# Performance work log

Hardware: AMD Instinct MI355X
Metric: run time of the kernel (lower is better)

## Reference

```python
import jax, jax.numpy as jnp
import numpy as np
from jax import lax

B, H, G, T = 16384, 128, 5, 12

def setup_inputs() -> dict:
    key = jax.random.key(0)
    ks = jax.random.split(key, 12)
    s = 0.05  # weight scale for numerical sanity
    return {
        "encoder_hidden": jax.random.normal(ks[0], (B, H), jnp.float32),
        "encoder_cell": jax.random.normal(ks[1], (B, H), jnp.float32),
        "last_position": jax.random.normal(ks[2], (B, 2), jnp.float32),
        "gp_w1": jax.random.normal(ks[3], (H, H), jnp.float32) * s,
        "gp_b1": jnp.zeros((H,), jnp.float32),
        "gp_w2": jax.random.normal(ks[4], (H, G * 2), jnp.float32) * s,
        "gp_b2": jnp.zeros((G * 2,), jnp.float32),
        "pr_w1": jax.random.normal(ks[5], (H, H // 2), jnp.float32) * s,
        "pr_b1": jnp.zeros((H // 2,), jnp.float32),
        "pr_w2": jax.random.normal(ks[6], (H // 2, G), jnp.float32) * s,
        "pr_b2": jnp.zeros((G,), jnp.float32),
        "w_ih": jax.random.normal(ks[7], (4, 4 * H), jnp.float32) * s,   # LSTM input weights [in=4, 4H] (i,f,g,o)
        "w_hh": jax.random.normal(ks[8], (H, 4 * H), jnp.float32) * s,   # LSTM recurrent weights [H, 4H]
        "b_ih": jnp.zeros((4 * H,), jnp.float32),
        "b_hh": jnp.zeros((4 * H,), jnp.float32),
        "ph_w": jax.random.normal(ks[9], (H, 2), jnp.float32) * s,
        "ph_b": jnp.zeros((2,), jnp.float32),
    }

def reference(encoder_hidden, encoder_cell, last_position,
              gp_w1, gp_b1, gp_w2, gp_b2,
              pr_w1, pr_b1, pr_w2, pr_b2,
              w_ih, w_hh, b_ih, b_hh, ph_w, ph_b):
    b = encoder_hidden.shape[0]
    # goal prediction: residual on last_position
    g_hid = jax.nn.relu(encoder_hidden @ gp_w1 + gp_b1)
    goals = (g_hid @ gp_w2 + gp_b2).reshape(b, G, 2) + last_position[:, None, :]  # [B,G,2]
    # goal probabilities
    p_hid = jax.nn.relu(encoder_hidden @ pr_w1 + pr_b1)
    goal_probs = jax.nn.softmax(p_hid @ pr_w2 + pr_b2, axis=-1)  # [B,G]
    # batch all goals together: leading goal dim [G,B,...]
    goals_gb = jnp.swapaxes(goals, 0, 1)                      # [G,B,2]
    h0 = jnp.broadcast_to(encoder_hidden, (G, b, H))
    c0 = jnp.broadcast_to(encoder_cell, (G, b, H))
    pos0 = jnp.broadcast_to(last_position, (G, b, 2))
    bias = b_ih + b_hh

    def step(carry, _):
        pos, h, c = carry
        x = jnp.concatenate([pos, goals_gb], axis=-1)          # [G,B,4]
        gates = x @ w_ih + h @ w_hh + bias                      # [G,B,4H]
        i, f, g, o = jnp.split(gates, 4, axis=-1)
        c_new = jax.nn.sigmoid(f) * c + jax.nn.sigmoid(i) * jnp.tanh(g)
        h_new = jax.nn.sigmoid(o) * jnp.tanh(c_new)
        pos_new = pos + (h_new @ ph_w + ph_b)                   # residual position update
        return (pos_new, h_new, c_new), pos_new

    _, path = lax.scan(step, (pos0, h0, c0), None, length=T)   # [T,G,B,2]
    predictions = jnp.transpose(path, (2, 1, 0, 3))            # [B,G,T,2]
    return predictions, goals, goal_probs
```

## Files before the change

### kernel.cpp

```cpp
#include <hip/hip_runtime.h>

#define Bn 16384
#define Hn 128
#define Gn 5
#define Tn 12

typedef __attribute__((ext_vector_type(8))) __bf16 bf16x8;
typedef __attribute__((ext_vector_type(4))) float f32x4;
typedef __attribute__((ext_vector_type(4))) unsigned int u32x4;
typedef __attribute__((ext_vector_type(2))) unsigned int u32x2;
typedef unsigned int u32;
typedef unsigned short u16;

#define MFMA(a, b, c) __builtin_amdgcn_mfma_f32_16x16x32_bf16((a), (b), (c), 0, 0, 0)

__device__ __forceinline__ u16 f2bf(float f) { return __builtin_bit_cast(u16, (__bf16)f); }
__device__ __forceinline__ float bf2f(u16 h) { u32 u = ((u32)h) << 16; return __builtin_bit_cast(float, u); }
__device__ __forceinline__ u32 pk2(float a, float b) { return (u32)f2bf(a) | ((u32)f2bf(b) << 16); }
__device__ __forceinline__ float sigf(float x) {
    return __builtin_amdgcn_rcpf(1.0f + __builtin_amdgcn_exp2f(-1.44269504f * x));
}
__device__ __forceinline__ float tanhf_(float x) {
    return 1.0f - 2.0f * __builtin_amdgcn_rcpf(1.0f + __builtin_amdgcn_exp2f(2.88539008f * x));
}

__device__ __forceinline__ int hbsw(int row, int bytein) {
    return row * 256 + ((((bytein >> 4) ^ row) & 15) << 4) + (bytein & 15);
}
__device__ __forceinline__ int pbsw(int row, int bytein) {
    return row * 128 + ((((bytein >> 4) ^ row) & 7) << 4) + (bytein & 15);
}

__global__ __launch_bounds__(256) void k_phaseA(
    const float* __restrict__ eh, const float* __restrict__ lastpos,
    const float* __restrict__ gp_w1, const float* __restrict__ gp_b1,
    const float* __restrict__ gp_w2, const float* __restrict__ gp_b2,
    const float* __restrict__ pr_w1, const float* __restrict__ pr_b1,
    const float* __restrict__ pr_w2, const float* __restrict__ pr_b2,
    float* __restrict__ goals_o, float* __restrict__ probs_o)
{
    __shared__ __align__(16) char eT[64 * 256];
    __shared__ __align__(16) char gT[64 * 256];
    __shared__ __align__(16) char pT[64 * 128];
    __shared__ float lgT[64 * 8];

    const int tid = threadIdx.x;
    const int lane = tid & 63;
    const int wv = tid >> 6;
    const int lg = lane >> 4, li = lane & 15;
    const int r0 = blockIdx.x * 64;
    const int rowbase = wv * 16;

    {
        int row = tid >> 2, seg = tid & 3;
        const float* src = eh + (size_t)(r0 + row) * Hn + seg * 32;
#pragma unroll
        for (int cc = 0; cc < 4; ++cc) {
            u32 p0 = pk2(src[cc * 8 + 0], src[cc * 8 + 1]);
            u32 p1 = pk2(src[cc * 8 + 2], src[cc * 8 + 3]);
            u32 p2 = pk2(src[cc * 8 + 4], src[cc * 8 + 5]);
            u32 p3 = pk2(src[cc * 8 + 6], src[cc * 8 + 7]);
            *(u32x4*)(eT + hbsw(row, seg * 64 + cc * 16)) = (u32x4){p0, p1, p2, p3};
        }
    }
    __syncthreads();

    bf16x8 Ae[4];
#pragma unroll
    for (int kc = 0; kc < 4; ++kc)
        Ae[kc] = *(const bf16x8*)(eT + hbsw(rowbase + li, kc * 64 + lg * 16));

#pragma unroll 1
    for (int nt = 0; nt < 8; ++nt) {
        int c1 = nt * 16 + li;
        f32x4 acc = {0.f, 0.f, 0.f, 0.f};
#pragma unroll
        for (int kc = 0; kc < 4; ++kc) {
            bf16x8 bfr;
#pragma unroll
            for (int j = 0; j < 8; ++j)
                bfr[j] = (__bf16)gp_w1[(size_t)(kc * 32 + lg * 8 + j) * Hn + c1];
            acc = MFMA(Ae[kc], bfr, acc);
        }
        float bias = gp_b1[c1];
#pragma unroll
        for (int r = 0; r < 4; ++r) {
            int row = rowbase + lg * 4 + r;
            float v = fmaxf(acc[r] + bias, 0.f);
            *(u16*)(gT + hbsw(row, c1 * 2)) = f2bf(v);
        }
    }
    __syncthreads();

    {
        bf16x8 Ag[4];
#pragma unroll
        for (int kc = 0; kc < 4; ++kc)
            Ag[kc] = *(const bf16x8*)(gT + hbsw(rowbase + li, kc * 64 + lg * 16));
        f32x4 acc = {0.f, 0.f, 0.f, 0.f};
#pragma unroll
        for (int kc = 0; kc < 4; ++kc) {
            bf16x8 bfr;
#pragma unroll
            for (int j = 0; j < 8; ++j) {
                int k = kc * 32 + lg * 8 + j;
                bfr[j] = (li < 10) ? (__bf16)gp_w2[k * 10 + li] : (__bf16)0.f;
            }
            acc = MFMA(Ag[kc], bfr, acc);
        }
        if (li < 10) {
            float b2 = gp_b2[li];
#pragma unroll
            for (int r = 0; r < 4; ++r) {
                int b = r0 + rowbase + lg * 4 + r;
                float v = acc[r] + b2 + lastpos[(size_t)b * 2 + (li & 1)];
                goals_o[(size_t)b * 10 + li] = v;
            }
        }
    }

#pragma unroll 1
    for (int nt = 0; nt < 4; ++nt) {
        int c1 = nt * 16 + li;
        f32x4 acc = {0.f, 0.f, 0.f, 0.f};
#pragma unroll
        for (int kc = 0; kc < 4; ++kc) {
            bf16x8 bfr;
#pragma unroll
            for (int j = 0; j < 8; ++j)
                bfr[j] = (__bf16)pr_w1[(size_t)(kc * 32 + lg * 8 + j) * 64 + c1];
            acc = MFMA(Ae[kc], bfr, acc);
        }
        float bias = pr_b1[c1];
#pragma unroll
        for (int r = 0; r < 4; ++r) {
            int row = rowbase + lg * 4 + r;
            float v = fmaxf(acc[r] + bias, 0.f);
            *(u16*)(pT + pbsw(row, c1 * 2)) = f2bf(v);
        }
    }
    __syncthreads();

    {
        bf16x8 Ap[2];
#pragma unroll
        for (int kc = 0; kc < 2; ++kc)
            Ap[kc] = *(const bf16x8*)(pT + pbsw(rowbase + li, kc * 64 + lg * 16));
        f32x4 acc = {0.f, 0.f, 0.f, 0.f};
#pragma unroll
        for (int kc = 0; kc < 2; ++kc) {
            bf16x8 bfr;
#pragma unroll
            for (int j = 0; j < 8; ++j) {
                int k = kc * 32 + lg * 8 + j;
                bfr[j] = (li < 5) ? (__bf16)pr_w2[k * 5 + li] : (__bf16)0.f;
            }
            acc = MFMA(Ap[kc], bfr, acc);
        }
        if (li < 5) {
            float b2 = pr_b2[li];
#pragma unroll
            for (int r = 0; r < 4; ++r) {
                int row = rowbase + lg * 4 + r;
                lgT[row * 8 + li] = acc[r] + b2;
            }
        }
    }
    __syncthreads();

    if (tid < 64) {
        int row = tid;
        float v0 = lgT[row * 8 + 0], v1 = lgT[row * 8 + 1], v2 = lgT[row * 8 + 2];
        float v3 = lgT[row * 8 + 3], v4 = lgT[row * 8 + 4];
        float mx = fmaxf(fmaxf(fmaxf(v0, v1), fmaxf(v2, v3)), v4);
        float e0 = __builtin_amdgcn_exp2f((v0 - mx) * 1.44269504f);
        float e1 = __builtin_amdgcn_exp2f((v1 - mx) * 1.44269504f);
        float e2 = __builtin_amdgcn_exp2f((v2 - mx) * 1.44269504f);
        float e3 = __builtin_amdgcn_exp2f((v3 - mx) * 1.44269504f);
        float e4 = __builtin_amdgcn_exp2f((v4 - mx) * 1.44269504f);
        float rs = __builtin_amdgcn_rcpf(e0 + e1 + e2 + e3 + e4);
        size_t ob = (size_t)(r0 + row) * 5;
        probs_o[ob + 0] = e0 * rs;
        probs_o[ob + 1] = e1 * rs;
        probs_o[ob + 2] = e2 * rs;
        probs_o[ob + 3] = e3 * rs;
        probs_o[ob + 4] = e4 * rs;
    }
}

__global__ __launch_bounds__(512) void k_lstm(
    const float* __restrict__ eh, const float* __restrict__ ec,
    const float* __restrict__ lastpos,
    const float* __restrict__ w_ih, const float* __restrict__ w_hh,
    const float* __restrict__ b_ih, const float* __restrict__ b_hh,
    const float* __restrict__ ph_w, const float* __restrict__ ph_b,
    const float* __restrict__ goals_o, float* __restrict__ preds)
{
    __shared__ __align__(16) char hT[2][64 * 256];

    const int tid = threadIdx.x;
    const int lane = tid & 63;
    const int wv = tid >> 6;
    const int lg = lane >> 4, li = lane & 15;
    const int r0 = blockIdx.x * 64;

    bf16x8 Wh[4][4];
    bf16x8 Wx[4];
#pragma unroll
    for (int gt = 0; gt < 4; ++gt) {
        const int cg = gt * 128 + wv * 16 + li;
#pragma unroll
        for (int kc = 0; kc < 4; ++kc) {
            bf16x8 f;
#pragma unroll
            for (int j = 0; j < 8; ++j)
                f[j] = (__bf16)w_hh[(size_t)(kc * 32 + lg * 8 + j) * 512 + cg];
            Wh[gt][kc] = f;
        }
        bf16x8 fx;
#pragma unroll
        for (int j = 0; j < 8; ++j) {
            int k = lg * 8 + j;
            float v = 0.f;
            if (k < 4) v = w_ih[k * 512 + cg];
            else if (k == 4) v = b_ih[cg] + b_hh[cg];
            fx[j] = (__bf16)v;
        }
        Wx[gt] = fx;
    }

    bf16x8 php[4];
#pragma unroll
    for (int kc = 0; kc < 4; ++kc) {
        u32 w[4];
#pragma unroll
        for (int jp = 0; jp < 4; ++jp) {
            int k = kc * 32 + lg * 8 + jp * 2;
            u32 xw = pk2(ph_w[k * 2 + 0], ph_w[k * 2 + 2]);
            u32 yw = pk2(ph_w[k * 2 + 1], ph_w[k * 2 + 3]);
            w[jp] = (li == 0) ? xw : yw;
        }
        php[kc] = __builtin_bit_cast(bf16x8, (u32x4){w[0], w[1], w[2], w[3]});
    }
    const float phb0 = ph_b[0], phb1 = ph_b[1];

    u32 gpk[4];
    float px[4], py[4];
#pragma unroll
    for (int m = 0; m < 4; ++m) {
        int gr = r0 + m * 16 + li;
        float2 g2 = *(const float2*)(goals_o + (size_t)gr * 2);
        gpk[m] = pk2(g2.x, g2.y);
        float2 p = *(const float2*)(lastpos + (size_t)(gr / 5) * 2);
        px[m] = p.x; py[m] = p.y;
    }

    const int ro0 = hbsw(li, 0 + lg * 16);
    const int ro1 = hbsw(li, 64 + lg * 16);
    const int ro2 = hbsw(li, 128 + lg * 16);
    const int ro3 = hbsw(li, 192 + lg * 16);
    const int wo  = hbsw(li, wv * 32 + lg * 8);

    {
        int row = tid >> 3, seg = tid & 7;
        int b = (r0 + row) / 5;
        const float* src = eh + (size_t)b * Hn + seg * 16;
#pragma unroll
        for (int cp = 0; cp < 2; ++cp) {
            u32 p0 = pk2(src[cp * 8 + 0], src[cp * 8 + 1]);
            u32 p1 = pk2(src[cp * 8 + 2], src[cp * 8 + 3]);
            u32 p2 = pk2(src[cp * 8 + 4], src[cp * 8 + 5]);
            u32 p3 = pk2(src[cp * 8 + 6], src[cp * 8 + 7]);
            *(u32x4*)(hT[0] + hbsw(row, seg * 32 + cp * 16)) = (u32x4){p0, p1, p2, p3};
        }
    }

    float c[4][4];
#pragma unroll
    for (int m = 0; m < 4; ++m) {
        int b = (r0 + m * 16 + li) / 5;
        float4 cv = *(const float4*)(ec + (size_t)b * Hn + wv * 16 + lg * 4);
        c[m][0] = cv.x; c[m][1] = cv.y; c[m][2] = cv.z; c[m][3] = cv.w;
    }

    __syncthreads();

#pragma unroll 1
    for (int t = 0; t < Tn; ++t) {
        const char* rbp = hT[0] + (t & 1) * 16384;
        char* wbp = hT[0] + ((t & 1) ^ 1) * 16384;
#pragma unroll
        for (int m = 0; m < 4; ++m) {
            const int mo = m * 4096;
            bf16x8 H0 = *(const bf16x8*)(rbp + ro0 + mo);
            bf16x8 H1 = *(const bf16x8*)(rbp + ro1 + mo);
            bf16x8 H2 = *(const bf16x8*)(rbp + ro2 + mo);
            bf16x8 H3 = *(const bf16x8*)(rbp + ro3 + mo);

            f32x4 a0 = {0.f, 0.f, 0.f, 0.f}, a1 = {0.f, 0.f, 0.f, 0.f};
            f32x4 a2 = {0.f, 0.f, 0.f, 0.f}, a3 = {0.f, 0.f, 0.f, 0.f};
            a0 = MFMA(Wh[0][0], H0, a0); a1 = MFMA(Wh[1][0], H0, a1);
            a2 = MFMA(Wh[2][0], H0, a2); a3 = MFMA(Wh[3][0], H0, a3);
            a0 = MFMA(Wh[0][1], H1, a0); a1 = MFMA(Wh[1][1], H1, a1);
            a2 = MFMA(Wh[2][1], H1, a2); a3 = MFMA(Wh[3][1], H1, a3);
            a0 = MFMA(Wh[0][2], H2, a0); a1 = MFMA(Wh[1][2], H2, a1);
            a2 = MFMA(Wh[2][2], H2, a2); a3 = MFMA(Wh[3][2], H2, a3);
            a0 = MFMA(Wh[0][3], H3, a0); a1 = MFMA(Wh[1][3], H3, a1);
            a2 = MFMA(Wh[2][3], H3, a2); a3 = MFMA(Wh[3][3], H3, a3);

            if (t > 0) {
                f32x4 pacc = {0.f, 0.f, 0.f, 0.f};
                pacc = MFMA(php[0], H0, pacc);
                pacc = MFMA(php[1], H1, pacc);
                pacc = MFMA(php[2], H2, pacc);
                pacc = MFMA(php[3], H3, pacc);
                px[m] += pacc[0] + phb0;
                py[m] += pacc[1] + phb1;
                if (wv == m && lg == 0) {
                    size_t o = ((size_t)(r0 + m * 16 + li) * Tn + (t - 1)) * 2;
                    *(float2*)(preds + o) = make_float2(px[m], py[m]);
                }
            }

            bf16x8 xf = __builtin_bit_cast(bf16x8,
                (u32x4){pk2(px[m], py[m]), gpk[m], 0x00003F80u, 0u});
            a0 = MFMA(Wx[0], xf, a0);
            a1 = MFMA(Wx[1], xf, a1);
            a2 = MFMA(Wx[2], xf, a2);
            a3 = MFMA(Wx[3], xf, a3);

            u32 w0, w1;
            {
                float cn0 = sigf(a1[0]) * c[m][0] + sigf(a0[0]) * tanhf_(a2[0]);
                float cn1 = sigf(a1[1]) * c[m][1] + sigf(a0[1]) * tanhf_(a2[1]);
                float cn2 = sigf(a1[2]) * c[m][2] + sigf(a0[2]) * tanhf_(a2[2]);
                float cn3 = sigf(a1[3]) * c[m][3] + sigf(a0[3]) * tanhf_(a2[3]);
                c[m][0] = cn0; c[m][1] = cn1; c[m][2] = cn2; c[m][3] = cn3;
                float h0 = sigf(a3[0]) * tanhf_(cn0);
                float h1 = sigf(a3[1]) * tanhf_(cn1);
                float h2 = sigf(a3[2]) * tanhf_(cn2);
                float h3 = sigf(a3[3]) * tanhf_(cn3);
                w0 = pk2(h0, h1);
                w1 = pk2(h2, h3);
            }
            *(u32x2*)(wbp + wo + mo) = (u32x2){w0, w1};
        }
        __syncthreads();
    }

    if (wv < 4) {
        const int m = wv;
        const char* rbp = hT[0];
        const int mo = m * 4096;
        bf16x8 H0 = *(const bf16x8*)(rbp + ro0 + mo);
        bf16x8 H1 = *(const bf16x8*)(rbp + ro1 + mo);
        bf16x8 H2 = *(const bf16x8*)(rbp + ro2 + mo);
        bf16x8 H3 = *(const bf16x8*)(rbp + ro3 + mo);
        f32x4 pacc = {0.f, 0.f, 0.f, 0.f};
        pacc = MFMA(php[0], H0, pacc);
        pacc = MFMA(php[1], H1, pacc);
        pacc = MFMA(php[2], H2, pacc);
        pacc = MFMA(php[3], H3, pacc);
        if (lg == 0) {
            float fx = px[m] + pacc[0] + phb0;
            float fy = py[m] + pacc[1] + phb1;
            size_t o = ((size_t)(r0 + m * 16 + li) * Tn + (Tn - 1)) * 2;
            *(float2*)(preds + o) = make_float2(fx, fy);
        }
    }
}

extern "C" void kernel_launch(void* const* d_in, const int* in_sizes, int n_in,
                              void* d_out, int out_size, void* d_ws, size_t ws_size,
                              hipStream_t stream)
{
    (void)in_sizes; (void)n_in; (void)out_size; (void)d_ws; (void)ws_size;
    const float* eh   = (const float*)d_in[0];
    const float* ec   = (const float*)d_in[1];
    const float* lp   = (const float*)d_in[2];
    const float* gpw1 = (const float*)d_in[3];
    const float* gpb1 = (const float*)d_in[4];
    const float* gpw2 = (const float*)d_in[5];
    const float* gpb2 = (const float*)d_in[6];
    const float* prw1 = (const float*)d_in[7];
    const float* prb1 = (const float*)d_in[8];
    const float* prw2 = (const float*)d_in[9];
    const float* prb2 = (const float*)d_in[10];
    const float* wih  = (const float*)d_in[11];
    const float* whh  = (const float*)d_in[12];
    const float* bih  = (const float*)d_in[13];
    const float* bhh  = (const float*)d_in[14];
    const float* phw  = (const float*)d_in[15];
    const float* phb  = (const float*)d_in[16];

    float* out = (float*)d_out;
    float* preds = out;
    float* goals = out + (size_t)Bn * Gn * Tn * 2;
    float* probs = out + (size_t)Bn * Gn * Tn * 2 + (size_t)Bn * Gn * 2;

    k_phaseA<<<Bn / 64, 256, 0, stream>>>(eh, lp, gpw1, gpb1, gpw2, gpb2,
                                          prw1, prb1, prw2, prb2, goals, probs);
    k_lstm<<<(Bn * Gn) / 64, 512, 0, stream>>>(eh, ec, lp, wih, whh, bih, bhh,
                                               phw, phb, goals, preds);
}
```

Before: 265.2 us.

## Enlarge LSTM block to 160 rows and fold activation scales into weights

Each LSTM block now processes 10 row tiles (160 rows) instead of 4. This amortizes the per-block register loading of W_hh/W_ih and cuts the block count from 1280 to 512. The log2e-based exponent scaling for the sigmoid and tanh gates is pre-multiplied into the bf16 weights and bias, removing a multiply per activation. The tradeoffs are more shared memory (80KB), which lowers occupancy, more registers for the c state, fewer blocks per CU, and a small bf16 rounding change from the scaled weights.

```diff
diff --git a/kernel.cpp b/kernel.cpp
--- a/kernel.cpp
+++ b/kernel.cpp
@@ -15,14 +15,7 @@
 #define MFMA(a, b, c) __builtin_amdgcn_mfma_f32_16x16x32_bf16((a), (b), (c), 0, 0, 0)
 
 __device__ __forceinline__ u16 f2bf(float f) { return __builtin_bit_cast(u16, (__bf16)f); }
-__device__ __forceinline__ float bf2f(u16 h) { u32 u = ((u32)h) << 16; return __builtin_bit_cast(float, u); }
 __device__ __forceinline__ u32 pk2(float a, float b) { return (u32)f2bf(a) | ((u32)f2bf(b) << 16); }
-__device__ __forceinline__ float sigf(float x) {
-    return __builtin_amdgcn_rcpf(1.0f + __builtin_amdgcn_exp2f(-1.44269504f * x));
-}
-__device__ __forceinline__ float tanhf_(float x) {
-    return 1.0f - 2.0f * __builtin_amdgcn_rcpf(1.0f + __builtin_amdgcn_exp2f(2.88539008f * x));
-}
 
 __device__ __forceinline__ int hbsw(int row, int bytein) {
     return row * 256 + ((((bytein >> 4) ^ row) & 15) << 4) + (bytein & 15);
@@ -196,25 +189,32 @@
     const float* __restrict__ ph_w, const float* __restrict__ ph_b,
     const float* __restrict__ goals_o, float* __restrict__ preds)
 {
-    __shared__ __align__(16) char hT[2][64 * 256];
+#define MT 10
+#define ROWS (MT * 16)
+#define BUFB (ROWS * 256)
+    __shared__ __align__(16) char hT[2][BUFB];
 
     const int tid = threadIdx.x;
     const int lane = tid & 63;
     const int wv = tid >> 6;
     const int lg = lane >> 4, li = lane & 15;
-    const int r0 = blockIdx.x * 64;
+    const int r0 = blockIdx.x * ROWS;
+
+    const float NL = -1.44269504f;
+    const float PG = 2.88539008f;
 
     bf16x8 Wh[4][4];
     bf16x8 Wx[4];
 #pragma unroll
     for (int gt = 0; gt < 4; ++gt) {
+        const float s = (gt == 2) ? PG : NL;
         const int cg = gt * 128 + wv * 16 + li;
 #pragma unroll
         for (int kc = 0; kc < 4; ++kc) {
             bf16x8 f;
 #pragma unroll
             for (int j = 0; j < 8; ++j)
-                f[j] = (__bf16)w_hh[(size_t)(kc * 32 + lg * 8 + j) * 512 + cg];
+                f[j] = (__bf16)(w_hh[(size_t)(kc * 32 + lg * 8 + j) * 512 + cg] * s);
             Wh[gt][kc] = f;
         }
         bf16x8 fx;
@@ -222,8 +222,8 @@
         for (int j = 0; j < 8; ++j) {
             int k = lg * 8 + j;
             float v = 0.f;
-            if (k < 4) v = w_ih[k * 512 + cg];
-            else if (k == 4) v = b_ih[cg] + b_hh[cg];
+            if (k < 4) v = w_ih[k * 512 + cg] * s;
+            else if (k == 4) v = (b_ih[cg] + b_hh[cg]) * s;
             fx[j] = (__bf16)v;
         }
         Wx[gt] = fx;
@@ -244,10 +244,10 @@
     }
     const float phb0 = ph_b[0], phb1 = ph_b[1];
 
-    u32 gpk[4];
-    float px[4], py[4];
-#pragma unroll
-    for (int m = 0; m < 4; ++m) {
+    u32 gpk[MT];
+    float px[MT], py[MT];
+#pragma unroll
+    for (int m = 0; m < MT; ++m) {
         int gr = r0 + m * 16 + li;
         float2 g2 = *(const float2*)(goals_o + (size_t)gr * 2);
         gpk[m] = pk2(g2.x, g2.y);
@@ -261,36 +261,34 @@
     const int ro3 = hbsw(li, 192 + lg * 16);
     const int wo  = hbsw(li, wv * 32 + lg * 8);
 
-    {
-        int row = tid >> 3, seg = tid & 7;
-        int b = (r0 + row) / 5;
-        const float* src = eh + (size_t)b * Hn + seg * 16;
-#pragma unroll
-        for (int cp = 0; cp < 2; ++cp) {
-            u32 p0 = pk2(src[cp * 8 + 0], src[cp * 8 + 1]);
-            u32 p1 = pk2(src[cp * 8 + 2], src[cp * 8 + 3]);
-            u32 p2 = pk2(src[cp * 8 + 4], src[cp * 8 + 5]);
-            u32 p3 = pk2(src[cp * 8 + 6], src[cp * 8 + 7]);
-            *(u32x4*)(hT[0] + hbsw(row, seg * 32 + cp * 16)) = (u32x4){p0, p1, p2, p3};
-        }
-    }
-
-    float c[4][4];
-#pragma unroll
-    for (int m = 0; m < 4; ++m) {
+#pragma unroll
+    for (int it = 0; it < 5; ++it) {
+        int chunk = tid + it * 512;
+        int row = chunk >> 4, seg = chunk & 15;
+        const float* src = eh + (size_t)((r0 + row) / 5) * Hn + seg * 8;
+        u32 p0 = pk2(src[0], src[1]);
+        u32 p1 = pk2(src[2], src[3]);
+        u32 p2 = pk2(src[4], src[5]);
+        u32 p3 = pk2(src[6], src[7]);
+        *(u32x4*)(hT[0] + hbsw(row, seg * 16)) = (u32x4){p0, p1, p2, p3};
+    }
+
+    f32x4 c[MT];
+#pragma unroll
+    for (int m = 0; m < MT; ++m) {
         int b = (r0 + m * 16 + li) / 5;
         float4 cv = *(const float4*)(ec + (size_t)b * Hn + wv * 16 + lg * 4);
-        c[m][0] = cv.x; c[m][1] = cv.y; c[m][2] = cv.z; c[m][3] = cv.w;
+        c[m] = (f32x4){cv.x, cv.y, cv.z, cv.w};
     }
 
     __syncthreads();
 
 #pragma unroll 1
     for (int t = 0; t < Tn; ++t) {
-        const char* rbp = hT[0] + (t & 1) * 16384;
-        char* wbp = hT[0] + ((t & 1) ^ 1) * 16384;
-#pragma unroll
-        for (int m = 0; m < 4; ++m) {
+        const char* rbp = hT[0] + (t & 1) * BUFB;
+        char* wbp = hT[0] + ((t & 1) ^ 1) * BUFB;
+#pragma unroll
+        for (int m = 0; m < MT; ++m) {
             const int mo = m * 4096;
             bf16x8 H0 = *(const bf16x8*)(rbp + ro0 + mo);
             bf16x8 H1 = *(const bf16x8*)(rbp + ro1 + mo);
@@ -316,7 +314,7 @@
                 pacc = MFMA(php[3], H3, pacc);
                 px[m] += pacc[0] + phb0;
                 py[m] += pacc[1] + phb1;
-                if (wv == m && lg == 0) {
+                if (((m & 7) == wv) && lg == 0) {
                     size_t o = ((size_t)(r0 + m * 16 + li) * Tn + (t - 1)) * 2;
                     *(float2*)(preds + o) = make_float2(px[m], py[m]);
                 }
@@ -331,25 +329,29 @@
 
             u32 w0, w1;
             {
-                float cn0 = sigf(a1[0]) * c[m][0] + sigf(a0[0]) * tanhf_(a2[0]);
-                float cn1 = sigf(a1[1]) * c[m][1] + sigf(a0[1]) * tanhf_(a2[1]);
-                float cn2 = sigf(a1[2]) * c[m][2] + sigf(a0[2]) * tanhf_(a2[2]);
-                float cn3 = sigf(a1[3]) * c[m][3] + sigf(a0[3]) * tanhf_(a2[3]);
-                c[m][0] = cn0; c[m][1] = cn1; c[m][2] = cn2; c[m][3] = cn3;
-                float h0 = sigf(a3[0]) * tanhf_(cn0);
-                float h1 = sigf(a3[1]) * tanhf_(cn1);
-                float h2 = sigf(a3[2]) * tanhf_(cn2);
-                float h3 = sigf(a3[3]) * tanhf_(cn3);
-                w0 = pk2(h0, h1);
-                w1 = pk2(h2, h3);
+                float hvv[4];
+#pragma unroll
+                for (int r = 0; r < 4; ++r) {
+                    float si = __builtin_amdgcn_rcpf(1.0f + __builtin_amdgcn_exp2f(a0[r]));
+                    float sf = __builtin_amdgcn_rcpf(1.0f + __builtin_amdgcn_exp2f(a1[r]));
+                    float tg = 1.0f - 2.0f * __builtin_amdgcn_rcpf(1.0f + __builtin_amdgcn_exp2f(a2[r]));
+                    float so = __builtin_amdgcn_rcpf(1.0f + __builtin_amdgcn_exp2f(a3[r]));
+                    float cn = sf * c[m][r] + si * tg;
+                    c[m][r] = cn;
+                    float tc = 1.0f - 2.0f * __builtin_amdgcn_rcpf(1.0f + __builtin_amdgcn_exp2f(PG * cn));
+                    hvv[r] = so * tc;
+                }
+                w0 = pk2(hvv[0], hvv[1]);
+                w1 = pk2(hvv[2], hvv[3]);
             }
             *(u32x2*)(wbp + wo + mo) = (u32x2){w0, w1};
         }
         __syncthreads();
     }
 
-    if (wv < 4) {
-        const int m = wv;
+#pragma unroll
+    for (int m = 0; m < MT; ++m) {
+        if ((m & 7) != wv) continue;
         const char* rbp = hT[0];
         const int mo = m * 4096;
         bf16x8 H0 = *(const bf16x8*)(rbp + ro0 + mo);
@@ -368,6 +370,9 @@
             *(float2*)(preds + o) = make_float2(fx, fy);
         }
     }
+#undef MT
+#undef ROWS
+#undef BUFB
 }
 
 extern "C" void kernel_launch(void* const* d_in, const int* in_sizes, int n_in,
@@ -400,6 +405,6 @@
 
     k_phaseA<<<Bn / 64, 256, 0, stream>>>(eh, lp, gpw1, gpb1, gpw2, gpb2,
                                           prw1, prb1, prw2, prb2, goals, probs);
-    k_lstm<<<(Bn * Gn) / 64, 512, 0, stream>>>(eh, ec, lp, wih, whh, bih, bhh,
-                                               phw, phb, goals, preds);
+    k_lstm<<<(Bn * Gn) / 160, 512, 0, stream>>>(eh, ec, lp, wih, whh, bih, bhh,
+                                                phw, phb, goals, preds);
 }
```

After: 246.5 us. 1.08x faster.
